# Performance work log

Measured on AMD Instinct MI355X. Metric: run time of the kernel, lower is better.

## Reference

```python
import jax, jax.numpy as jnp
import numpy as np

B, N = 4096, 2048


def setup_inputs() -> dict:
    key = jax.random.key(0)
    k1, k2, k3, k4 = jax.random.split(key, 4)
    return {
        "src_pts3d": jax.random.normal(k1, (B, N, 3), dtype=jnp.float32),
        "tgt_pts3d": jax.random.normal(k2, (B, N, 3), dtype=jnp.float32),
        "kpt_src_mask": jax.random.uniform(k3, (B, N), dtype=jnp.float32),
        "kpt_tgt_mask": jax.random.uniform(k4, (B, N), dtype=jnp.float32),
    }


def reference(src_pts3d, tgt_pts3d, kpt_src_mask, kpt_tgt_mask):
    # H = src^T @ diag(mask_tgt) @ tgt, fused as a masked row-scale contraction: [B,3,3]
    H = jnp.einsum('bnc,bn,bnd->bcd', src_pts3d, kpt_tgt_mask, tgt_pts3d)
    # torch.svd returns V (H = U S V^T); jnp returns Vh, so V = Vh^T
    u, s, vh = jnp.linalg.svd(H)
    v = jnp.swapaxes(vh, -1, -2)              # [B,3,3]
    ut = jnp.swapaxes(u, -1, -2)              # [B,3,3]
    r = v @ ut
    det = jnp.linalg.det(r)                   # [B]
    # branch-free reflection fix: negate 3rd column of V when det(r) < 0
    sign = jnp.where(det < 0, -1.0, 1.0)
    col_scale = jnp.stack([jnp.ones_like(sign), jnp.ones_like(sign), sign], axis=-1)  # [B,3]
    R = (v * col_scale[:, None, :]) @ ut
    return R
```

## Files before the change

kernel.cpp:

```cpp
#include <hip/hip_runtime.h>
#include <math.h>

#define BATCH 4096
#define NPTS  2048
#define THREADS 256
#define BPB 4
#define GRID (BATCH / BPB)

typedef float f32x4 __attribute__((ext_vector_type(4)));

__device__ __forceinline__ f32x4 ntload(const f32x4* p) {
    return __builtin_nontemporal_load(p);
}

#define ACC(sx, sy, sz, tx, ty, tz, mm) do {                                   \
    float d0 = (mm) * (tx), d1 = (mm) * (ty), d2 = (mm) * (tz);                \
    h[0] = fmaf((sx), d0, h[0]); h[1] = fmaf((sx), d1, h[1]); h[2] = fmaf((sx), d2, h[2]); \
    h[3] = fmaf((sy), d0, h[3]); h[4] = fmaf((sy), d1, h[4]); h[5] = fmaf((sy), d2, h[5]); \
    h[6] = fmaf((sz), d0, h[6]); h[7] = fmaf((sz), d1, h[7]); h[8] = fmaf((sz), d2, h[8]); \
} while (0)

#define DECL_HALF(P) f32x4 P##m, P##sa, P##sb, P##sc, P##ta, P##tb, P##tc;

#define LOAD_HALF(P, bb, g) do {                                               \
    const f32x4* s4_ = (const f32x4*)(src  + (size_t)(bb) * (NPTS * 3));       \
    const f32x4* t4_ = (const f32x4*)(tgt  + (size_t)(bb) * (NPTS * 3));       \
    const f32x4* m4_ = (const f32x4*)(mask + (size_t)(bb) * NPTS);             \
    const int g_ = (g);                                                        \
    P##m  = ntload(&m4_[g_]);                                                  \
    P##sa = ntload(&s4_[3 * g_ + 0]);                                          \
    P##sb = ntload(&s4_[3 * g_ + 1]);                                          \
    P##sc = ntload(&s4_[3 * g_ + 2]);                                          \
    P##ta = ntload(&t4_[3 * g_ + 0]);                                          \
    P##tb = ntload(&t4_[3 * g_ + 1]);                                          \
    P##tc = ntload(&t4_[3 * g_ + 2]);                                          \
} while (0)

#define FMA_HALF(P) do {                                                       \
    ACC(P##sa.x, P##sa.y, P##sa.z, P##ta.x, P##ta.y, P##ta.z, P##m.x);         \
    ACC(P##sa.w, P##sb.x, P##sb.y, P##ta.w, P##tb.x, P##tb.y, P##m.y);         \
    ACC(P##sb.z, P##sb.w, P##sc.x, P##tb.z, P##tb.w, P##tc.x, P##m.z);         \
    ACC(P##sc.y, P##sc.z, P##sc.w, P##tc.y, P##tc.z, P##tc.w, P##m.w);         \
} while (0)

__device__ __attribute__((noinline))
void solve_one(float f0, float f1, float f2, float f3, float f4, float f5,
               float f6, float f7, float f8, float* __restrict__ o)
{
    double H[3][3] = {{(double)f0, (double)f1, (double)f2},
                      {(double)f3, (double)f4, (double)f5},
                      {(double)f6, (double)f7, (double)f8}};

    double A[3][3];
#pragma unroll
    for (int i = 0; i < 3; ++i)
#pragma unroll
        for (int j = 0; j < 3; ++j)
            A[i][j] = H[0][i] * H[0][j] + H[1][i] * H[1][j] + H[2][i] * H[2][j];

    double V[3][3] = {{1, 0, 0}, {0, 1, 0}, {0, 0, 1}};

    for (int sweep = 0; sweep < 6; ++sweep) {
#pragma unroll
        for (int r = 0; r < 3; ++r) {
            const int p = (r == 2) ? 1 : 0;
            const int q = (r == 0) ? 1 : 2;
            const int k = (r == 0) ? 2 : ((r == 1) ? 1 : 0);
            double apq = A[p][q];
            if (fabs(apq) > 1e-300) {
                double theta = (A[q][q] - A[p][p]) / (2.0 * apq);
                double tt = 1.0 / (fabs(theta) + sqrt(theta * theta + 1.0));
                if (theta < 0.0) tt = -tt;
                double c = 1.0 / sqrt(tt * tt + 1.0);
                double s = tt * c;
                double app = A[p][p], aqq = A[q][q];
                A[p][p] = app - tt * apq;
                A[q][q] = aqq + tt * apq;
                A[p][q] = A[q][p] = 0.0;
                double akp = A[k][p], akq = A[k][q];
                A[k][p] = A[p][k] = c * akp - s * akq;
                A[k][q] = A[q][k] = s * akp + c * akq;
#pragma unroll
                for (int i = 0; i < 3; ++i) {
                    double vip = V[i][p], viq = V[i][q];
                    V[i][p] = c * vip - s * viq;
                    V[i][q] = s * vip + c * viq;
                }
            }
        }
    }

    const double d0 = A[0][0], d1 = A[1][1], d2 = A[2][2];
    const bool g01 = (d0 >= d1);
    const bool g02 = (d0 >= d2);
    const bool g12 = (d1 >= d2);
    const bool l0 = g01 && g02;
    const bool l1 = (!g01) && g12;

    double v0[3], v1[3];
#pragma unroll
    for (int i = 0; i < 3; ++i) {
        const double c0 = V[i][0], c1 = V[i][1], c2 = V[i][2];
        v0[i] = l0 ? c0 : (l1 ? c1 : c2);
        const double s_l0 = g12 ? c1 : c2;
        const double s_l1 = g02 ? c0 : c2;
        const double s_l2 = g01 ? c0 : c1;
        v1[i] = l0 ? s_l0 : (l1 ? s_l1 : s_l2);
    }

    double b0[3], b1[3];
#pragma unroll
    for (int r = 0; r < 3; ++r) {
        b0[r] = H[r][0] * v0[0] + H[r][1] * v0[1] + H[r][2] * v0[2];
        b1[r] = H[r][0] * v1[0] + H[r][1] * v1[1] + H[r][2] * v1[2];
    }
    double n0 = b0[0] * b0[0] + b0[1] * b0[1] + b0[2] * b0[2];
    double inv0 = 1.0 / sqrt(fmax(n0, 1e-300));
    double u0[3] = {b0[0] * inv0, b0[1] * inv0, b0[2] * inv0};
    double d01 = u0[0] * b1[0] + u0[1] * b1[1] + u0[2] * b1[2];
    double w[3] = {b1[0] - d01 * u0[0], b1[1] - d01 * u0[1], b1[2] - d01 * u0[2]};
    double nw = w[0] * w[0] + w[1] * w[1] + w[2] * w[2];
    double inv1 = 1.0 / sqrt(fmax(nw, 1e-300));
    double u1[3] = {w[0] * inv1, w[1] * inv1, w[2] * inv1};
    double u2[3] = {u0[1] * u1[2] - u0[2] * u1[1],
                    u0[2] * u1[0] - u0[0] * u1[2],
                    u0[0] * u1[1] - u0[1] * u1[0]};
    double vc2[3] = {v0[1] * v1[2] - v0[2] * v1[1],
                     v0[2] * v1[0] - v0[0] * v1[2],
                     v0[0] * v1[1] - v0[1] * v1[0]};

#pragma unroll
    for (int r = 0; r < 3; ++r)
#pragma unroll
        for (int c = 0; c < 3; ++c)
            o[r * 3 + c] = (float)(v0[r] * u0[c] + v1[r] * u1[c] + vc2[r] * u2[c]);
}

__global__ __launch_bounds__(THREADS, 4)
void fused_kernel(const float* __restrict__ src, const float* __restrict__ tgt,
                  const float* __restrict__ mask, float* __restrict__ out)
{
    const int t    = threadIdx.x;
    const int b0   = blockIdx.x * BPB;
    const int wid  = t >> 6;
    const int lane = t & 63;

    __shared__ float shred[2][THREADS / 64][9];

    DECL_HALF(A0) DECL_HALF(A1) DECL_HALF(B_)

#define HS(jj, i) (shred[(jj) & 1][0][i] + shred[(jj) & 1][1][i] + \
                   shred[(jj) & 1][2][i] + shred[(jj) & 1][3][i])

#define ITER(CUR, NXT, jj, DO_PREF) do {                                       \
    LOAD_HALF(B_, b0 + (jj), t + 256);                                         \
    float h[9] = {0.f, 0.f, 0.f, 0.f, 0.f, 0.f, 0.f, 0.f, 0.f};               \
    FMA_HALF(CUR);                                                             \
    if (DO_PREF) { LOAD_HALF(NXT, b0 + (jj) + 1, t); }                         \
    FMA_HALF(B_);                                                              \
    _Pragma("unroll")                                                          \
    for (int off = 32; off > 0; off >>= 1) {                                   \
        _Pragma("unroll")                                                      \
        for (int i = 0; i < 9; ++i) h[i] += __shfl_down(h[i], off);            \
    }                                                                          \
    if (lane == 0) {                                                           \
        _Pragma("unroll")                                                      \
        for (int i = 0; i < 9; ++i) shred[(jj) & 1][wid][i] = h[i];            \
    }                                                                          \
    __syncthreads();                                                           \
    if (t == 0) {                                                              \
        solve_one(HS(jj, 0), HS(jj, 1), HS(jj, 2),                             \
                  HS(jj, 3), HS(jj, 4), HS(jj, 5),                             \
                  HS(jj, 6), HS(jj, 7), HS(jj, 8),                             \
                  out + (size_t)(b0 + (jj)) * 9);                              \
    }                                                                          \
} while (0)

    LOAD_HALF(A0, b0, t);
    ITER(A0, A1, 0, 1);
    ITER(A1, A0, 1, 1);
    ITER(A0, A1, 2, 1);
    ITER(A1, A0, 3, 0);

#undef ITER
#undef HS
}

extern "C" void kernel_launch(void* const* d_in, const int* in_sizes, int n_in,
                              void* d_out, int out_size, void* d_ws, size_t ws_size,
                              hipStream_t stream) {
    const float* src  = (const float*)d_in[0];
    const float* tgt  = (const float*)d_in[1];
    const float* mask = (const float*)d_in[3];
    float* out = (float*)d_out;

    fused_kernel<<<GRID, THREADS, 0, stream>>>(src, tgt, mask, out);
}
```

Baseline: 252.0 us.

## Defer per-batch 3x3 SVD solves to one parallel phase after all reductions

Instead of a syncthreads plus a serial single-thread SVD after each of the four batches, all four partial reductions are written to separate shared slots, followed by one barrier, and then four threads (one per batch) solve in parallel. The Jacobi rotation branch is made branch-free with selects so that the four lanes do not diverge. This takes the serialized double-precision solves off the critical path and cuts the barriers from four to one. In exchange, the solves now sit at the end of the block instead of overlapping with the loads for the next batch, and the branch-free form always runs the rotation arithmetic.

Result: faster. 246.1 us (-2.3%).

```diff
diff --git a/kernel.cpp b/kernel.cpp
--- a/kernel.cpp
+++ b/kernel.cpp
@@ -43,13 +43,52 @@
     ACC(P##sc.y, P##sc.z, P##sc.w, P##tc.y, P##tc.z, P##tc.w, P##m.w);         \
 } while (0)
 
-__device__ __attribute__((noinline))
-void solve_one(float f0, float f1, float f2, float f3, float f4, float f5,
-               float f6, float f7, float f8, float* __restrict__ o)
+__global__ __launch_bounds__(THREADS, 4)
+void fused_kernel(const float* __restrict__ src, const float* __restrict__ tgt,
+                  const float* __restrict__ mask, float* __restrict__ out)
 {
-    double H[3][3] = {{(double)f0, (double)f1, (double)f2},
-                      {(double)f3, (double)f4, (double)f5},
-                      {(double)f6, (double)f7, (double)f8}};
+    const int t    = threadIdx.x;
+    const int b0   = blockIdx.x * BPB;
+    const int wid  = t >> 6;
+    const int lane = t & 63;
+
+    __shared__ float shred[BPB][THREADS / 64][9];
+
+    DECL_HALF(A0) DECL_HALF(A1) DECL_HALF(B_)
+
+#define ITER(CUR, NXT, jj, DO_PREF) do {                                       \
+    LOAD_HALF(B_, b0 + (jj), t + 256);                                         \
+    float h[9] = {0.f, 0.f, 0.f, 0.f, 0.f, 0.f, 0.f, 0.f, 0.f};               \
+    FMA_HALF(CUR);                                                             \
+    if (DO_PREF) { LOAD_HALF(NXT, b0 + (jj) + 1, t); }                         \
+    FMA_HALF(B_);                                                              \
+    _Pragma("unroll")                                                          \
+    for (int off = 32; off > 0; off >>= 1) {                                   \
+        _Pragma("unroll")                                                      \
+        for (int i = 0; i < 9; ++i) h[i] += __shfl_down(h[i], off);            \
+    }                                                                          \
+    if (lane == 0) {                                                           \
+        _Pragma("unroll")                                                      \
+        for (int i = 0; i < 9; ++i) shred[jj][wid][i] = h[i];                  \
+    }                                                                          \
+} while (0)
+
+    LOAD_HALF(A0, b0, t);
+    ITER(A0, A1, 0, 1);
+    ITER(A1, A0, 1, 1);
+    ITER(A0, A1, 2, 1);
+    ITER(A1, A0, 3, 0);
+#undef ITER
+
+    __syncthreads();
+
+    if (t >= BPB) return;
+
+    double H[3][3];
+#pragma unroll
+    for (int i = 0; i < 9; ++i)
+        H[i / 3][i % 3] = (double)(shred[t][0][i] + shred[t][1][i] +
+                                   shred[t][2][i] + shred[t][3][i]);
 
     double A[3][3];
 #pragma unroll
@@ -67,25 +106,25 @@
             const int q = (r == 0) ? 1 : 2;
             const int k = (r == 0) ? 2 : ((r == 1) ? 1 : 0);
             double apq = A[p][q];
-            if (fabs(apq) > 1e-300) {
-                double theta = (A[q][q] - A[p][p]) / (2.0 * apq);
-                double tt = 1.0 / (fabs(theta) + sqrt(theta * theta + 1.0));
-                if (theta < 0.0) tt = -tt;
-                double c = 1.0 / sqrt(tt * tt + 1.0);
-                double s = tt * c;
-                double app = A[p][p], aqq = A[q][q];
-                A[p][p] = app - tt * apq;
-                A[q][q] = aqq + tt * apq;
-                A[p][q] = A[q][p] = 0.0;
-                double akp = A[k][p], akq = A[k][q];
-                A[k][p] = A[p][k] = c * akp - s * akq;
-                A[k][q] = A[q][k] = s * akp + c * akq;
+            const bool nz = fabs(apq) > 1e-300;
+            double theta = (A[q][q] - A[p][p]) / (nz ? 2.0 * apq : 1.0);
+            double tt = 1.0 / (fabs(theta) + sqrt(theta * theta + 1.0));
+            tt = (theta < 0.0) ? -tt : tt;
+            tt = nz ? tt : 0.0;
+            double c = 1.0 / sqrt(tt * tt + 1.0);
+            double s = tt * c;
+            double app = A[p][p], aqq = A[q][q];
+            A[p][p] = app - tt * apq;
+            A[q][q] = aqq + tt * apq;
+            A[p][q] = A[q][p] = 0.0;
+            double akp = A[k][p], akq = A[k][q];
+            A[k][p] = A[p][k] = c * akp - s * akq;
+            A[k][q] = A[q][k] = s * akp + c * akq;
 #pragma unroll
-                for (int i = 0; i < 3; ++i) {
-                    double vip = V[i][p], viq = V[i][q];
-                    V[i][p] = c * vip - s * viq;
-                    V[i][q] = s * vip + c * viq;
-                }
+            for (int i = 0; i < 3; ++i) {
+                double vip = V[i][p], viq = V[i][q];
+                V[i][p] = c * vip - s * viq;
+                V[i][q] = s * vip + c * viq;
             }
         }
     }
@@ -108,17 +147,17 @@
         v1[i] = l0 ? s_l0 : (l1 ? s_l1 : s_l2);
     }
 
-    double b0[3], b1[3];
+    double b0v[3], b1v[3];
 #pragma unroll
     for (int r = 0; r < 3; ++r) {
-        b0[r] = H[r][0] * v0[0] + H[r][1] * v0[1] + H[r][2] * v0[2];
-        b1[r] = H[r][0] * v1[0] + H[r][1] * v1[1] + H[r][2] * v1[2];
+        b0v[r] = H[r][0] * v0[0] + H[r][1] * v0[1] + H[r][2] * v0[2];
+        b1v[r] = H[r][0] * v1[0] + H[r][1] * v1[1] + H[r][2] * v1[2];
     }
-    double n0 = b0[0] * b0[0] + b0[1] * b0[1] + b0[2] * b0[2];
+    double n0 = b0v[0] * b0v[0] + b0v[1] * b0v[1] + b0v[2] * b0v[2];
     double inv0 = 1.0 / sqrt(fmax(n0, 1e-300));
-    double u0[3] = {b0[0] * inv0, b0[1] * inv0, b0[2] * inv0};
-    double d01 = u0[0] * b1[0] + u0[1] * b1[1] + u0[2] * b1[2];
-    double w[3] = {b1[0] - d01 * u0[0], b1[1] - d01 * u0[1], b1[2] - d01 * u0[2]};
+    double u0[3] = {b0v[0] * inv0, b0v[1] * inv0, b0v[2] * inv0};
+    double d01 = u0[0] * b1v[0] + u0[1] * b1v[1] + u0[2] * b1v[2];
+    double w[3] = {b1v[0] - d01 * u0[0], b1v[1] - d01 * u0[1], b1v[2] - d01 * u0[2]};
     double nw = w[0] * w[0] + w[1] * w[1] + w[2] * w[2];
     double inv1 = 1.0 / sqrt(fmax(nw, 1e-300));
     double u1[3] = {w[0] * inv1, w[1] * inv1, w[2] * inv1};
@@ -129,61 +168,12 @@
                      v0[2] * v1[0] - v0[0] * v1[2],
                      v0[0] * v1[1] - v0[1] * v1[0]};
 
+    float* o = out + (size_t)(b0 + t) * 9;
 #pragma unroll
     for (int r = 0; r < 3; ++r)
 #pragma unroll
         for (int c = 0; c < 3; ++c)
             o[r * 3 + c] = (float)(v0[r] * u0[c] + v1[r] * u1[c] + vc2[r] * u2[c]);
-}
-
-__global__ __launch_bounds__(THREADS, 4)
-void fused_kernel(const float* __restrict__ src, const float* __restrict__ tgt,
-                  const float* __restrict__ mask, float* __restrict__ out)
-{
-    const int t    = threadIdx.x;
-    const int b0   = blockIdx.x * BPB;
-    const int wid  = t >> 6;
-    const int lane = t & 63;
-
-    __shared__ float shred[2][THREADS / 64][9];
-
-    DECL_HALF(A0) DECL_HALF(A1) DECL_HALF(B_)
-
-#define HS(jj, i) (shred[(jj) & 1][0][i] + shred[(jj) & 1][1][i] + \
-                   shred[(jj) & 1][2][i] + shred[(jj) & 1][3][i])
-
-#define ITER(CUR, NXT, jj, DO_PREF) do {                                       \
-    LOAD_HALF(B_, b0 + (jj), t + 256);                                         \
-    float h[9] = {0.f, 0.f, 0.f, 0.f, 0.f, 0.f, 0.f, 0.f, 0.f};               \
-    FMA_HALF(CUR);                                                             \
-    if (DO_PREF) { LOAD_HALF(NXT, b0 + (jj) + 1, t); }                         \
-    FMA_HALF(B_);                                                              \
-    _Pragma("unroll")                                                          \
-    for (int off = 32; off > 0; off >>= 1) {                                   \
-        _Pragma("unroll")                                                      \
-        for (int i = 0; i < 9; ++i) h[i] += __shfl_down(h[i], off);            \
-    }                                                                          \
-    if (lane == 0) {                                                           \
-        _Pragma("unroll")                                                      \
-        for (int i = 0; i < 9; ++i) shred[(jj) & 1][wid][i] = h[i];            \
-    }                                                                          \
-    __syncthreads();                                                           \
-    if (t == 0) {                                                              \
-        solve_one(HS(jj, 0), HS(jj, 1), HS(jj, 2),                             \
-                  HS(jj, 3), HS(jj, 4), HS(jj, 5),                             \
-                  HS(jj, 6), HS(jj, 7), HS(jj, 8),                             \
-                  out + (size_t)(b0 + (jj)) * 9);                              \
-    }                                                                          \
-} while (0)
-
-    LOAD_HALF(A0, b0, t);
-    ITER(A0, A1, 0, 1);
-    ITER(A1, A0, 1, 1);
-    ITER(A0, A1, 2, 1);
-    ITER(A1, A0, 3, 0);
-
-#undef ITER
-#undef HS
 }
 
 extern "C" void kernel_launch(void* const* d_in, const int* in_sizes, int n_in,
```
